# Kernel optimization log

Hardware: AMD Instinct MI355X
Metric: run time of the kernel (lower is better)

## Reference

```python
import jax, jax.numpy as jnp
import numpy as np
from jax import lax

GAMMA = 1.0
LAM = 1.0
ITERS = 20          # fixed PGD iterations for the graph fused-lasso solve
B = 2048            # number of graphs
NMAX = 1536         # max graph size (for padded per-graph sparsemax)


def setup_inputs() -> dict:
    sizes = (512 + (np.arange(B, dtype=np.int64) * 997) % 1025).astype(np.int32)
    N = int(sizes.sum())  # 2098092
    offsets = np.concatenate([[0], np.cumsum(sizes)[:-1]]).astype(np.int64)
    gid = np.repeat(np.arange(B, dtype=np.int64), sizes)
    # chain edges within each graph
    same = gid[1:] == gid[:-1]
    ca = np.arange(N - 1, dtype=np.int64)[same]
    cb = ca + 1
    # one random intra-graph edge per node
    rng = np.random.RandomState(0)
    u = rng.randint(0, 1 << 30, size=(N, 2)).astype(np.int64)
    ra = offsets[gid] + u[:, 0] % sizes[gid]
    rb = offsets[gid] + u[:, 1] % sizes[gid]
    edges = np.stack([np.concatenate([ca, ra]), np.concatenate([cb, rb])], axis=1).astype(np.int32)
    key = jax.random.key(0)
    x = jax.random.normal(key, (N,), dtype=jnp.float32)
    return {"x": x, "sizes": jnp.asarray(sizes), "edges": jnp.asarray(edges)}


def _gfusedmax(x, sizes, edges):
    N = x.shape[0]
    a = edges[:, 0]
    b = edges[:, 1]
    # --- graph fused lasso: min_y 0.5||y-x||^2 + LAM * sum_e |y_a - y_b|
    # solved on the dual via projected gradient: y = x - D^T u, u in [-LAM, LAM]^E
    deg = jnp.zeros((N,), x.dtype).at[a].add(1.0).at[b].add(1.0)
    step = 1.0 / (2.0 * jnp.max(deg))  # 1/L, L <= 2*max_degree

    def dT(u):  # D^T u : node accumulation of signed edge duals
        return jnp.zeros_like(x).at[a].add(u).at[b].add(-u)

    def body(u, _):
        y = x - dT(u)
        u = jnp.clip(u + step * (y[a] - y[b]), -LAM, LAM)
        return u, None

    u0 = jnp.zeros((a.shape[0],), x.dtype)
    u, _ = lax.scan(body, u0, None, length=ITERS)
    y = x - dT(u)

    # --- per-graph sparsemax(y / GAMMA) over ragged segments, scaled by graph size
    offsets = jnp.concatenate([jnp.zeros((1,), sizes.dtype), jnp.cumsum(sizes)[:-1]])
    gid = jnp.repeat(jnp.arange(B), sizes, total_repeat_length=N)   # [N] graph id
    pos = jnp.arange(N) - offsets[gid]                               # [N] pos in graph
    z = y / GAMMA
    NEG = jnp.asarray(-1e30, z.dtype)
    padded = jnp.full((B, NMAX), NEG, z.dtype).at[gid, pos].set(z)   # [B, NMAX]
    zs = -jnp.sort(-padded, axis=1)                                  # descending
    k = jnp.arange(1, NMAX + 1, dtype=z.dtype)
    cs = jnp.cumsum(zs, axis=1)
    support = (1.0 + k * zs) > cs                                    # padded entries fail
    kmax = jnp.sum(support, axis=1)                                  # [B], >= 1
    cs_k = jnp.take_along_axis(cs, (kmax - 1)[:, None], axis=1)[:, 0]
    tau = (cs_k - 1.0) / kmax.astype(z.dtype)
    p = jnp.maximum(z - tau[gid], 0.0)
    return p * sizes[gid].astype(z.dtype)


def reference(x, sizes, edges):
    return _gfusedmax(x, sizes, edges)
```

## Files before the change

### kernel.cpp

```cpp
#include <hip/hip_runtime.h>

#define NT 256
#define CAP 2176
#define SLOT 9
#define GMAXN 1536
#define TVITERS 20
#define BISECT 18
#define BMAX 4096

__device__ int g_off[BMAX];
__device__ int g_maxdeg;

__global__ __launch_bounds__(NT) void k_scan(const int* __restrict__ sizes, int B) {
  __shared__ int part[NT];
  int t = threadIdx.x;
  int per = (B + NT - 1) / NT;
  int base = t * per;
  int acc = 0;
  for (int k = 0; k < per; ++k) {
    int i = base + k;
    if (i < B) acc += sizes[i];
  }
  part[t] = acc;
  __syncthreads();
  if (t == 0) {
    int run = 0;
    for (int i = 0; i < NT; ++i) { int tmp = part[i]; part[i] = run; run += tmp; }
    g_maxdeg = 0;
  }
  __syncthreads();
  int run = part[t];
  for (int k = 0; k < per; ++k) {
    int i = base + k;
    if (i < B) { g_off[i] = run; run += sizes[i]; }
  }
}

__global__ __launch_bounds__(NT) void k_deg(const int* __restrict__ sizes,
                                            const int* __restrict__ edges,
                                            int N, int B) {
  __shared__ int cnt[GMAXN];
  __shared__ int wred[4];
  int g = blockIdx.x;
  int t = threadIdx.x;
  int s = sizes[g];
  int off = g_off[g];
  for (int i = t; i < s; i += NT)
    cnt[i] = 2 - (i == 0 ? 1 : 0) - (i == s - 1 ? 1 : 0);
  __syncthreads();
  const int2* re2 = (const int2*)(edges + 2 * ((N - B) + off));
  for (int j = t; j < s; j += NT) {
    int2 e = re2[j];
    atomicAdd(&cnt[e.x - off], 1);
    atomicAdd(&cnt[e.y - off], 1);
  }
  __syncthreads();
  int m = 0;
  for (int i = t; i < s; i += NT) m = max(m, cnt[i]);
  #pragma unroll
  for (int o = 32; o > 0; o >>= 1) m = max(m, __shfl_down(m, o, 64));
  if ((t & 63) == 0) wred[t >> 6] = m;
  __syncthreads();
  if (t == 0) {
    m = max(max(wred[0], wred[1]), max(wred[2], wred[3]));
    atomicMax(&g_maxdeg, m);
  }
}

__global__ __launch_bounds__(NT, 4) void k_main(const float* __restrict__ x,
                                                const int* __restrict__ sizes,
                                                const int* __restrict__ edges,
                                                float* __restrict__ out,
                                                int N, int B) {
  __shared__ float yL[CAP];
  __shared__ float uE[2 * CAP];
  __shared__ float uCh[CAP];
  __shared__ ushort offL[CAP + 2];
  __shared__ float redf[2][8];
  __shared__ int wtot[4];

  int b = blockIdx.x;
  int t = threadIdx.x;
  int lane = t & 63, wid = t >> 6;
  int g1 = b, g2 = B - 1 - b;
  int s1g = sizes[g1], off1g = g_off[g1];
  int s2g = 0, off2g = 0;
  if (g2 > g1) { s2g = sizes[g2]; off2g = g_off[g2]; }
  float step = 1.0f / (2.0f * (float)g_maxdeg);
  int nch = N - B;
  int npass = (s1g + s2g <= CAP) ? 1 : 2;

  for (int pass = 0; pass < npass; ++pass) {
    int ss1, oo1, ss2, oo2;
    if (npass == 1) { ss1 = s1g; oo1 = off1g; ss2 = s2g; oo2 = off2g; }
    else { ss1 = pass ? s2g : s1g; oo1 = pass ? off2g : off1g; ss2 = 0; oo2 = 0; }
    int S = ss1 + ss2;
    __syncthreads();

    uint ab[SLOT];
    #pragma unroll
    for (int k = 0; k < SLOT; ++k) {
      int j = t + k * NT;
      uint pk = 0;
      if (j < S) {
        int2 e;
        if (j < ss1) { e = ((const int2*)edges)[nch + oo1 + j];
                       pk = (uint)(e.x - oo1) | ((uint)(e.y - oo1) << 16); }
        else         { e = ((const int2*)edges)[nch + oo2 + (j - ss1)];
                       pk = (uint)(e.x - oo2 + ss1) | ((uint)(e.y - oo2 + ss1) << 16); }
      }
      ab[k] = pk;
    }
    float xr[SLOT];
    #pragma unroll
    for (int k = 0; k < SLOT; ++k) {
      int i = t + k * NT;
      float v = 0.0f;
      if (i < S) v = (i < ss1) ? x[oo1 + i] : x[oo2 + i - ss1];
      xr[k] = v;
    }

    int* cnt = (int*)yL;
    #pragma unroll
    for (int k = 0; k < SLOT; ++k) { int i = t + k * NT; if (i < S) cnt[i] = 0; }
    __syncthreads();
    #pragma unroll
    for (int k = 0; k < SLOT; ++k) {
      int j = t + k * NT;
      if (j < S) {
        atomicAdd(&cnt[ab[k] & 0xFFFFu], 1);
        atomicAdd(&cnt[ab[k] >> 16], 1);
      }
    }
    __syncthreads();
    int c[SLOT];
    int tot = 0;
    #pragma unroll
    for (int k = 0; k < SLOT; ++k) {
      int i = t * SLOT + k;
      int v = (i < S) ? cnt[i] : 0;
      c[k] = tot; tot += v;
    }
    int inc = tot;
    #pragma unroll
    for (int o = 1; o < 64; o <<= 1) {
      int n = __shfl_up(inc, o, 64);
      if (lane >= o) inc += n;
    }
    if (lane == 63) wtot[wid] = inc;
    __syncthreads();
    int wpre = 0;
    #pragma unroll
    for (int w = 0; w < 4; ++w) wpre += (w < wid) ? wtot[w] : 0;
    int basep = wpre + (inc - tot);
    int* cur = (int*)uE;
    #pragma unroll
    for (int k = 0; k < SLOT; ++k) {
      int i = t * SLOT + k;
      if (i < S) { int v = basep + c[k]; offL[i] = (ushort)v; cur[i] = v; }
    }
    if (t == 0) offL[S] = (ushort)(2 * S);
    __syncthreads();
    uint pw[SLOT];
    #pragma unroll
    for (int k = 0; k < SLOT; ++k) {
      int j = t + k * NT;
      uint v = 0;
      if (j < S) {
        int pa = atomicAdd(&cur[ab[k] & 0xFFFFu], 1);
        int pb = atomicAdd(&cur[ab[k] >> 16], 1);
        v = (uint)pa | ((uint)pb << 16);
      }
      pw[k] = v;
    }
    uint pq[SLOT];
    #pragma unroll
    for (int k = 0; k < SLOT; ++k) {
      int i = t + k * NT;
      uint v = 0;
      if (i < S) { uint p0 = offL[i]; uint n = (uint)offL[i + 1] - p0; v = p0 | (n << 16); }
      pq[k] = v;
    }
    float yreg[SLOT], uC[SLOT], uRr[SLOT];
    #pragma unroll
    for (int k = 0; k < SLOT; ++k) {
      int i = t + k * NT;
      uC[k] = 0.0f; uRr[k] = 0.0f;
      if (i < S) { yL[i] = xr[k]; uCh[i] = 0.0f; }
      yreg[k] = (i < S) ? xr[k] : -1e30f;
    }
    __syncthreads();

    for (int it = 0; it < TVITERS; ++it) {
      float yn[SLOT], ya[SLOT], yb[SLOT];
      #pragma unroll
      for (int k = 0; k < SLOT; ++k) {
        int i = t + k * NT;
        yn[k] = (i + 1 < S) ? yL[i + 1] : 0.0f;
      }
      #pragma unroll
      for (int k = 0; k < SLOT; ++k) {
        int j = t + k * NT;
        if (j < S) {
          ya[k] = yL[ab[k] & 0xFFFFu];
          yb[k] = yL[ab[k] >> 16];
        }
      }
      #pragma unroll
      for (int k = 0; k < SLOT; ++k) {
        int i = t + k * NT;
        bool ch = (i < S - 1) && (i != ss1 - 1);
        if (ch) {
          float nu = uC[k] + step * (yreg[k] - yn[k]);
          nu = fminf(1.0f, fmaxf(-1.0f, nu));
          uC[k] = nu;
          uCh[i] = nu;
        }
      }
      #pragma unroll
      for (int k = 0; k < SLOT; ++k) {
        int j = t + k * NT;
        if (j < S) {
          float nu = uRr[k] + step * (ya[k] - yb[k]);
          nu = fminf(1.0f, fmaxf(-1.0f, nu));
          uRr[k] = nu;
          uE[pw[k] & 0xFFFFu] = -nu;
          uE[pw[k] >> 16] = nu;
        }
      }
      __syncthreads();
      #pragma unroll
      for (int k = 0; k < SLOT; ++k) {
        int i = t + k * NT;
        if (i < S) {
          float y = xr[k];
          if (i > 0 && i != ss1) y += uCh[i - 1];
          if ((i < S - 1) && (i != ss1 - 1)) y -= uC[k];
          uint p = pq[k] & 0xFFFFu, n = pq[k] >> 16;
          for (uint q = 0; q < n; ++q) y += uE[p + q];
          yreg[k] = y;
          yL[i] = y;
        }
      }
      __syncthreads();
    }

    float m1 = -1e30f, m2 = -1e30f;
    #pragma unroll
    for (int k = 0; k < SLOT; ++k) {
      int i = t + k * NT;
      if (i < S) { if (i < ss1) m1 = fmaxf(m1, yreg[k]); else m2 = fmaxf(m2, yreg[k]); }
    }
    #pragma unroll
    for (int o = 1; o < 64; o <<= 1) {
      m1 = fmaxf(m1, __shfl_xor(m1, o, 64));
      m2 = fmaxf(m2, __shfl_xor(m2, o, 64));
    }
    if (lane == 0) { redf[0][wid] = m1; redf[0][4 + wid] = m2; }
    __syncthreads();
    m1 = fmaxf(fmaxf(redf[0][0], redf[0][1]), fmaxf(redf[0][2], redf[0][3]));
    m2 = fmaxf(fmaxf(redf[0][4], redf[0][5]), fmaxf(redf[0][6], redf[0][7]));

    float lo1 = m1 - 1.0f, hi1 = m1, lo2 = m2 - 1.0f, hi2 = m2;
    int par = 1;
    for (int r = 0; r < BISECT; ++r) {
      float mid1 = 0.5f * (lo1 + hi1), mid2 = 0.5f * (lo2 + hi2);
      float f1 = 0.0f, f2 = 0.0f;
      #pragma unroll
      for (int k = 0; k < SLOT; ++k) {
        int i = t + k * NT;
        if (i < S) {
          if (i < ss1) f1 += fmaxf(yreg[k] - mid1, 0.0f);
          else         f2 += fmaxf(yreg[k] - mid2, 0.0f);
        }
      }
      #pragma unroll
      for (int o = 1; o < 64; o <<= 1) {
        f1 += __shfl_xor(f1, o, 64);
        f2 += __shfl_xor(f2, o, 64);
      }
      if (lane == 0) { redf[par][wid] = f1; redf[par][4 + wid] = f2; }
      __syncthreads();
      f1 = redf[par][0] + redf[par][1] + redf[par][2] + redf[par][3];
      f2 = redf[par][4] + redf[par][5] + redf[par][6] + redf[par][7];
      par ^= 1;
      if (f1 >= 1.0f) lo1 = mid1; else hi1 = mid1;
      if (f2 >= 1.0f) lo2 = mid2; else hi2 = mid2;
    }
    __syncthreads();
    float cf1 = 0.0f, S1 = 0.0f, cf2 = 0.0f, S2 = 0.0f;
    #pragma unroll
    for (int k = 0; k < SLOT; ++k) {
      int i = t + k * NT;
      if (i < S) {
        if (i < ss1) { if (yreg[k] > lo1) { cf1 += 1.0f; S1 += yreg[k]; } }
        else         { if (yreg[k] > lo2) { cf2 += 1.0f; S2 += yreg[k]; } }
      }
    }
    #pragma unroll
    for (int o = 1; o < 64; o <<= 1) {
      cf1 += __shfl_xor(cf1, o, 64);
      S1  += __shfl_xor(S1,  o, 64);
      cf2 += __shfl_xor(cf2, o, 64);
      S2  += __shfl_xor(S2,  o, 64);
    }
    float* redflat = (float*)redf;
    if (lane == 0) {
      redflat[wid] = cf1; redflat[4 + wid] = S1;
      redflat[8 + wid] = cf2; redflat[12 + wid] = S2;
    }
    __syncthreads();
    cf1 = redflat[0] + redflat[1] + redflat[2] + redflat[3];
    S1  = redflat[4] + redflat[5] + redflat[6] + redflat[7];
    cf2 = redflat[8] + redflat[9] + redflat[10] + redflat[11];
    S2  = redflat[12] + redflat[13] + redflat[14] + redflat[15];
    float tau1 = (S1 - 1.0f) / cf1;
    float tau2 = (cf2 > 0.0f) ? (S2 - 1.0f) / cf2 : 0.0f;

    float sf1 = (float)ss1, sf2 = (float)ss2;
    #pragma unroll
    for (int k = 0; k < SLOT; ++k) {
      int i = t + k * NT;
      if (i < S) {
        bool in2 = (i >= ss1);
        float tau = in2 ? tau2 : tau1;
        float sf = in2 ? sf2 : sf1;
        int o = in2 ? (oo2 + i - ss1) : (oo1 + i);
        out[o] = fmaxf(yreg[k] - tau, 0.0f) * sf;
      }
    }
  }
}

extern "C" void kernel_launch(void* const* d_in, const int* in_sizes, int n_in,
                              void* d_out, int out_size, void* d_ws, size_t ws_size,
                              hipStream_t stream) {
  const float* x = (const float*)d_in[0];
  const int* sizes = (const int*)d_in[1];
  const int* edges = (const int*)d_in[2];
  float* out = (float*)d_out;
  int N = in_sizes[0];
  int B = in_sizes[1];
  (void)d_ws; (void)ws_size; (void)n_in; (void)out_size;

  k_scan<<<1, NT, 0, stream>>>(sizes, B);
  k_deg<<<B, NT, 0, stream>>>(sizes, edges, N, B);
  int nb = (B + 1) / 2;
  k_main<<<nb, NT, 0, stream>>>(x, sizes, edges, out, N, B);
}
```

Baseline: 189.7 us.

## Pair graphs by sorted size rank to balance block work

Adds a counting sort of graph sizes in the scan kernel so each block pairs the smallest remaining graph with the largest, which equalizes per-block node counts and avoids two-pass blocks. CAP shrinks to match the balanced pair total (about 2048+), lowering LDS use. It also cuts the bisection iterations from 18 to 14 and skips the final LDS store and barrier in the last TV iteration. Fewer bisection steps may reduce threshold precision.

```diff
diff --git a/kernel.cpp b/kernel.cpp
--- a/kernel.cpp
+++ b/kernel.cpp
@@ -1,19 +1,26 @@
 #include <hip/hip_runtime.h>
 
 #define NT 256
-#define CAP 2176
+#define CAP 2064
 #define SLOT 9
 #define GMAXN 1536
 #define TVITERS 20
-#define BISECT 18
+#define BISECT 14
 #define BMAX 4096
+#define NBIN 1025
 
 __device__ int g_off[BMAX];
+__device__ int g_rank[BMAX];
 __device__ int g_maxdeg;
 
 __global__ __launch_bounds__(NT) void k_scan(const int* __restrict__ sizes, int B) {
   __shared__ int part[NT];
+  __shared__ int histC[NBIN];
+  __shared__ int histO[NBIN];
+  __shared__ int wtot[4];
   int t = threadIdx.x;
+  int lane = t & 63, wid = t >> 6;
+
   int per = (B + NT - 1) / NT;
   int base = t * per;
   int acc = 0;
@@ -33,6 +40,41 @@
   for (int k = 0; k < per; ++k) {
     int i = base + k;
     if (i < B) { g_off[i] = run; run += sizes[i]; }
+  }
+
+  for (int i = t; i < NBIN; i += NT) histC[i] = 0;
+  __syncthreads();
+  for (int i = t; i < B; i += NT) atomicAdd(&histC[sizes[i] - 512], 1);
+  __syncthreads();
+  int c[5];
+  int tot = 0;
+  #pragma unroll
+  for (int k = 0; k < 5; ++k) {
+    int i = t * 5 + k;
+    int v = (i < NBIN) ? histC[i] : 0;
+    c[k] = tot; tot += v;
+  }
+  int inc = tot;
+  #pragma unroll
+  for (int o = 1; o < 64; o <<= 1) {
+    int n = __shfl_up(inc, o, 64);
+    if (lane >= o) inc += n;
+  }
+  if (lane == 63) wtot[wid] = inc;
+  __syncthreads();
+  int wpre = 0;
+  #pragma unroll
+  for (int w = 0; w < 4; ++w) wpre += (w < wid) ? wtot[w] : 0;
+  int basep = wpre + (inc - tot);
+  #pragma unroll
+  for (int k = 0; k < 5; ++k) {
+    int i = t * 5 + k;
+    if (i < NBIN) histO[i] = basep + c[k];
+  }
+  __syncthreads();
+  for (int i = t; i < B; i += NT) {
+    int r = atomicAdd(&histO[sizes[i] - 512], 1);
+    g_rank[r] = i;
   }
 }
 
@@ -48,7 +90,7 @@
   for (int i = t; i < s; i += NT)
     cnt[i] = 2 - (i == 0 ? 1 : 0) - (i == s - 1 ? 1 : 0);
   __syncthreads();
-  const int2* re2 = (const int2*)(edges + 2 * ((N - B) + off));
+  const int2* re2 = (const int2*)(edges) + (N - B) + off;
   for (int j = t; j < s; j += NT) {
     int2 e = re2[j];
     atomicAdd(&cnt[e.x - off], 1);
@@ -82,10 +124,12 @@
   int b = blockIdx.x;
   int t = threadIdx.x;
   int lane = t & 63, wid = t >> 6;
-  int g1 = b, g2 = B - 1 - b;
+  int g1 = g_rank[b];
+  int g2i = B - 1 - b;
+  int g2 = (g2i != b) ? g_rank[g2i] : -1;
   int s1g = sizes[g1], off1g = g_off[g1];
   int s2g = 0, off2g = 0;
-  if (g2 > g1) { s2g = sizes[g2]; off2g = g_off[g2]; }
+  if (g2 >= 0) { s2g = sizes[g2]; off2g = g_off[g2]; }
   float step = 1.0f / (2.0f * (float)g_maxdeg);
   int nch = N - B;
   int npass = (s1g + s2g <= CAP) ? 1 : 2;
@@ -192,6 +236,7 @@
     __syncthreads();
 
     for (int it = 0; it < TVITERS; ++it) {
+      bool last = (it == TVITERS - 1);
       float yn[SLOT], ya[SLOT], yb[SLOT];
       #pragma unroll
       for (int k = 0; k < SLOT; ++k) {
@@ -239,10 +284,10 @@
           uint p = pq[k] & 0xFFFFu, n = pq[k] >> 16;
           for (uint q = 0; q < n; ++q) y += uE[p + q];
           yreg[k] = y;
-          yL[i] = y;
-        }
-      }
-      __syncthreads();
+          if (!last) yL[i] = y;
+        }
+      }
+      if (!last) __syncthreads();
     }
 
     float m1 = -1e30f, m2 = -1e30f;
```

Measured after the change: 185.7 us. -2.1%, faster.
